# Kernel optimization log

Hardware: AMD Instinct MI355X
Metric: run time of the kernel (lower is better)

Reference implementation:

```python
import jax, jax.numpy as jnp
import numpy as np

H = 8          # n_heads
LORA_SCALE = 1.0


def _lora(x, down, up):
    # nn.Linear convention: y = x @ W.T ; down:[r,in], up:[out,r]
    return (x @ down.T) @ up.T


def setup_inputs() -> dict:
    key = jax.random.key(0)
    ks = jax.random.split(key, 16)
    B, S, D, R = 4, 2048, 640, 4
    std = 1.0 / np.sqrt(D)
    inp = {
        "hidden_states": jax.random.normal(ks[0], (B, S, D), jnp.float32),
        "wq": jax.random.normal(ks[1], (D, D), jnp.float32) * std,
        "wk": jax.random.normal(ks[2], (D, D), jnp.float32) * std,
        "wv": jax.random.normal(ks[3], (D, D), jnp.float32) * std,
        "wo": jax.random.normal(ks[4], (D, D), jnp.float32) * std,
        "bo": jax.random.normal(ks[5], (D,), jnp.float32) * 0.02,
        "q_down": jax.random.normal(ks[6], (R, D), jnp.float32) * (1.0 / R),
        "q_up": jax.random.normal(ks[7], (D, R), jnp.float32) * 0.02,
        "k_down": jax.random.normal(ks[8], (R, D), jnp.float32) * (1.0 / R),
        "k_up": jax.random.normal(ks[9], (D, R), jnp.float32) * 0.02,
        "v_down": jax.random.normal(ks[10], (R, D), jnp.float32) * (1.0 / R),
        "v_up": jax.random.normal(ks[11], (D, R), jnp.float32) * 0.02,
        "o_down": jax.random.normal(ks[12], (R, D), jnp.float32) * (1.0 / R),
        "o_up": jax.random.normal(ks[13], (D, R), jnp.float32) * 0.02,
    }
    return inp


def reference(hidden_states, wq, wk, wv, wo, bo,
              q_down, q_up, k_down, k_up, v_down, v_up, o_down, o_up):
    B, S, D = hidden_states.shape
    hd = D // H
    sm_scale = 1.0 / np.sqrt(hd)

    x = hidden_states  # self-attention: encoder_hidden_states = hidden_states
    q = x @ wq.T + LORA_SCALE * _lora(x, q_down, q_up)
    k = x @ wk.T + LORA_SCALE * _lora(x, k_down, k_up)
    v = x @ wv.T + LORA_SCALE * _lora(x, v_down, v_up)

    # head_to_batch_dim: [B,S,D] -> [B,H,S,hd]
    q = q.reshape(B, S, H, hd).transpose(0, 2, 1, 3)
    k = k.reshape(B, S, H, hd).transpose(0, 2, 1, 3)
    v = v.reshape(B, S, H, hd).transpose(0, 2, 1, 3)

    # get_attention_scores: baddbmm(beta=0, alpha=1/sqrt(hd)) + softmax
    scores = jnp.einsum("bhqd,bhkd->bhqk", q, k) * sm_scale
    probs = jax.nn.softmax(scores, axis=-1)
    attn_out = jnp.einsum("bhqk,bhkd->bhqd", probs, v)

    # batch_to_head_dim: [B,H,S,hd] -> [B,S,D]
    attn_out = attn_out.transpose(0, 2, 1, 3).reshape(B, S, D)

    # out projection (with bias) + LoRA on the pre-projection hidden states
    out = attn_out @ wo.T + bo + LORA_SCALE * _lora(attn_out, o_down, o_up)
    # to_out[1] is dropout -> identity at eval
    return out
```

## Files before the change

kernel.cpp:

```cpp
#include <hip/hip_runtime.h>

typedef unsigned short u16;
typedef unsigned int u32;
typedef unsigned long long u64;

typedef __bf16 bf16x8 __attribute__((ext_vector_type(8)));
typedef float f32x4 __attribute__((ext_vector_type(4)));
typedef float f32x16 __attribute__((ext_vector_type(16)));

__device__ __forceinline__ float b2f(u16 u) {
    union { u32 i; float f; } c; c.i = ((u32)u) << 16; return c.f;
}
__device__ __forceinline__ u16 f2b(float f) {
    union { float f; u32 i; } c; c.f = f;
    u32 r = c.i + 0x7fffu + ((c.i >> 16) & 1u);
    return (u16)(r >> 16);
}
__device__ __forceinline__ u32 cvt_pk_bf16(float a, float b) {
    u32 r;
    asm("v_cvt_pk_bf16_f32 %0, %1, %2" : "=v"(r) : "v"(a), "v"(b));
    return r;
}
__device__ __forceinline__ float fexp2(float x) {
    float r;
    asm("v_exp_f32 %0, %1" : "=v"(r) : "v"(x));
    return r;
}

__device__ __forceinline__ f32x4 mfma16(bf16x8 a, bf16x8 b, f32x4 c) {
    return __builtin_amdgcn_mfma_f32_16x16x32_bf16(a, b, c, 0, 0, 0);
}
__device__ __forceinline__ f32x16 mfma32(bf16x8 a, bf16x8 b, f32x16 c) {
    return __builtin_amdgcn_mfma_f32_32x32x16_bf16(a, b, c, 0, 0, 0);
}

__device__ __forceinline__ void lds_cp16(const u16* gsrc, u16* ldst) {
    __builtin_amdgcn_global_load_lds(
        (const __attribute__((address_space(1))) u32*)gsrc,
        (__attribute__((address_space(3))) u32*)ldst, 16, 0, 0);
}

struct ConvJobs {
    const float* s[4];
    u16* d[4];
};

__global__ __launch_bounds__(256) void convert_w(ConvJobs J) {
    int j = blockIdx.y;
    int i = blockIdx.x * 256 + threadIdx.x;
    float4 v = ((const float4*)J.s[j])[i];
    ushort4 o;
    o.x = f2b(v.x); o.y = f2b(v.y); o.z = f2b(v.z); o.w = f2b(v.w);
    ((ushort4*)J.d[j])[i] = o;
}

__global__ __launch_bounds__(256) void fuse_x(const float* __restrict__ x,
                                              const float* __restrict__ qd,
                                              const float* __restrict__ kd,
                                              const float* __restrict__ vd,
                                              u16* __restrict__ xb,
                                              float* __restrict__ T) {
    int m = blockIdx.x * 4 + (threadIdx.x >> 6);
    int lane = threadIdx.x & 63;
    const float* row = x + (size_t)m * 640;
    u16* orow = xb + (size_t)m * 640;
    float acc[12];
#pragma unroll
    for (int r = 0; r < 12; ++r) acc[r] = 0.f;
#pragma unroll
    for (int ii = 0; ii < 10; ++ii) {
        int i = lane + ii * 64;
        float a = row[i];
        orow[i] = f2b(a);
#pragma unroll
        for (int r = 0; r < 4; ++r) {
            acc[r]     += a * qd[r * 640 + i];
            acc[4 + r] += a * kd[r * 640 + i];
            acc[8 + r] += a * vd[r * 640 + i];
        }
    }
#pragma unroll
    for (int off = 32; off > 0; off >>= 1)
#pragma unroll
        for (int r = 0; r < 12; ++r) acc[r] += __shfl_xor(acc[r], off);
    if (lane == 0) {
#pragma unroll
        for (int p = 0; p < 3; ++p) {
            float4* t = (float4*)(T + ((size_t)p * 8192 + m) * 4);
            *t = make_float4(acc[p * 4], acc[p * 4 + 1], acc[p * 4 + 2], acc[p * 4 + 3]);
        }
    }
}

__global__ __launch_bounds__(256) void lora_down_o(const u16* __restrict__ A,
                                                   const float* __restrict__ dn,
                                                   float* __restrict__ T) {
    int m = blockIdx.x * 4 + (threadIdx.x >> 6);
    int lane = threadIdx.x & 63;
    const u16* arow = A + (size_t)m * 640;
    float a0 = 0.f, a1 = 0.f, a2 = 0.f, a3 = 0.f;
    for (int i = lane; i < 640; i += 64) {
        float a = b2f(arow[i]);
        a0 += a * dn[i];
        a1 += a * dn[640 + i];
        a2 += a * dn[1280 + i];
        a3 += a * dn[1920 + i];
    }
#pragma unroll
    for (int off = 32; off > 0; off >>= 1) {
        a0 += __shfl_xor(a0, off);
        a1 += __shfl_xor(a1, off);
        a2 += __shfl_xor(a2, off);
        a3 += __shfl_xor(a3, off);
    }
    if (lane == 0) {
        float4* t = (float4*)(T + (size_t)m * 4);
        *t = make_float4(a0, a1, a2, a3);
    }
}

struct QkvPtrs {
    const u16* W[3];
    const float* up[3];
    void* out[3];
    float scale[3];
};

__global__ __launch_bounds__(256) void gemm_bt(const u16* __restrict__ A, QkvPtrs P,
                                               const float* __restrict__ T,
                                               const float* __restrict__ bias, int mode) {
    int z = blockIdx.z;
    const u16* W = P.W[z];
    const float* up = P.up[z];
    const float scl = P.scale[z];
    const float* Tz = T + (size_t)z * 8192 * 4;
    int m0 = blockIdx.x * 128, n0 = blockIdx.y * 128;
    int tid = threadIdx.x, lane = tid & 63, wid = tid >> 6;
    int g = lane >> 4, l15 = lane & 15;
    __shared__ __align__(16) u16 As[128 * 32];
    __shared__ __align__(16) u16 Bs[128 * 32];
    f32x4 acc[4][4] = {};
    int wm = (wid & 1) * 64, wn = (wid >> 1) * 64;

    for (int k0 = 0; k0 < 640; k0 += 32) {
        __syncthreads();
#pragma unroll
        for (int it = 0; it < 2; ++it) {
            int f = tid + it * 256;
            int r = f >> 2, c = f & 3;
            lds_cp16(A + (size_t)(m0 + r) * 640 + k0 + c * 8, As + f * 8);
            lds_cp16(W + (size_t)(n0 + r) * 640 + k0 + c * 8, Bs + f * 8);
        }
        __syncthreads();
        bf16x8 af[4], bfv[4];
#pragma unroll
        for (int t = 0; t < 4; ++t) {
            af[t] = *(const bf16x8*)(As + (wm + t * 16 + l15) * 32 + g * 8);
            bfv[t] = *(const bf16x8*)(Bs + (wn + t * 16 + l15) * 32 + g * 8);
        }
#pragma unroll
        for (int i = 0; i < 4; ++i)
#pragma unroll
            for (int j = 0; j < 4; ++j)
                acc[i][j] = mfma16(af[i], bfv[j], acc[i][j]);
    }

    float4 upv[4];
    float bv[4];
#pragma unroll
    for (int j = 0; j < 4; ++j) {
        int n = n0 + wn + j * 16 + l15;
        upv[j] = *(const float4*)(up + n * 4);
        bv[j] = mode ? bias[n] : 0.f;
    }
    float* outf = (float*)P.out[z];
    u16* outb = (u16*)P.out[z];
#pragma unroll
    for (int i = 0; i < 4; ++i) {
#pragma unroll
        for (int r = 0; r < 4; ++r) {
            int m = m0 + wm + i * 16 + g * 4 + r;
            const float4 tv = *(const float4*)(Tz + (size_t)m * 4);
#pragma unroll
            for (int j = 0; j < 4; ++j) {
                int n = n0 + wn + j * 16 + l15;
                float v = acc[i][j][r] + tv.x * upv[j].x + tv.y * upv[j].y +
                          tv.z * upv[j].z + tv.w * upv[j].w + bv[j];
                if (mode) {
                    outf[(size_t)m * 640 + n] = v;
                } else {
                    int bb = m >> 11, s = m & 2047;
                    int h = n / 80, d = n - h * 80;
                    outb[(((size_t)bb * 8 + h) * 2048 + s) * 80 + d] = f2b(v * scl);
                }
            }
        }
    }
}

__global__ __launch_bounds__(256) void transpose_v(const u16* __restrict__ Vin,
                                                   u16* __restrict__ Vout) {
    __shared__ u32 lds32[64 * 41];
    int bh = blockIdx.y;
    int s0 = blockIdx.x * 64;
    int tid = threadIdx.x;
    const u16* in = Vin + (size_t)bh * 2048 * 80;
    u16* out = Vout + (size_t)bh * 96 * 2048;

    for (int t = tid; t < 640; t += 256) {
        int s = t / 10, c = t - s * 10;
        uint4 v = *(const uint4*)(in + (size_t)(s0 + s) * 80 + c * 8);
        u32* p = lds32 + s * 41 + c * 4;
        p[0] = v.x; p[1] = v.y; p[2] = v.z; p[3] = v.w;
    }
    __syncthreads();
    for (int t = tid; t < 640; t += 256) {
        int d = t >> 3, c8 = t & 7;
        int dp = d >> 1, hi = d & 1;
        u16 vals[8];
#pragma unroll
        for (int j = 0; j < 8; ++j) {
            u32 w = lds32[(c8 * 8 + j) * 41 + dp];
            vals[j] = hi ? (u16)(w >> 16) : (u16)(w & 0xffff);
        }
        u16* dst = out + (size_t)d * 2048 + s0 + (c8 >> 1) * 16 + (c8 & 1) * 4;
        *(uint2*)dst = *(const uint2*)(vals);
        *(uint2*)(dst + 8) = *(const uint2*)(vals + 4);
    }
    for (int t = tid; t < 1024; t += 256) {
        int r = t >> 6, c = t & 63;
        out[(size_t)(80 + r) * 2048 + s0 + c] = (r == 0) ? 0x3F80 : 0;
    }
}

__global__ __launch_bounds__(512) void flash_attn(const u16* __restrict__ Q,
                                                  const u16* __restrict__ K,
                                                  const u16* __restrict__ Vt_g,
                                                  u16* __restrict__ O) {
    int bh = blockIdx.y;
    int q0 = blockIdx.x * 256;
    int tid = threadIdx.x;
    int lane = tid & 63, wid = tid >> 6, l31 = lane & 31, h2 = lane >> 5;
    const size_t base = (size_t)bh * 2048 * 80;
    const size_t vbase = (size_t)bh * 96 * 2048;

    __shared__ __align__(16) u16 lds[2 * 5632 + 2 * 7200];
    u16* Ks0 = lds;
    u16* Vt0 = lds + 11264;

    bf16x8 qf[5];
    {
        int qrow = q0 + wid * 32 + l31;
#pragma unroll
        for (int ks = 0; ks < 5; ++ks)
            qf[ks] = *(const bf16x8*)(Q + base + (size_t)qrow * 80 + ks * 16 + h2 * 8);
    }

    f32x16 oa[3] = {};
    const float C2 = 17.312340490667562f;

    auto stage = [&](int buf, int kt) {
#pragma unroll
        for (int it = 0; it < 4; ++it) {
            int c = tid + it * 512;
            if (c < 704) {
                int row = c / 11, col = c - row * 11;
                lds_cp16(K + base + (size_t)(kt + row) * 80 + col * 8,
                         Ks0 + buf * 5632 + c * 8);
            } else if (c < 1600) {
                int t = c - 704;
                int row = t / 9, col = t - row * 9;
                lds_cp16(Vt_g + vbase + (size_t)row * 2048 + kt + col * 8,
                         Vt0 + buf * 7200 + t * 8);
            }
        }
    };

    stage(0, 0);
    __syncthreads();

    for (int i = 0; i < 32; ++i) {
        int cur = i & 1;
        if (i < 31) stage(cur ^ 1, (i + 1) * 64);

        const u16* ks = Ks0 + cur * 5632;
        const u16* vt = Vt0 + cur * 7200;

#pragma unroll
        for (int kk2 = 0; kk2 < 2; ++kk2) {
            f32x16 s = {};
#pragma unroll
            for (int ks5 = 0; ks5 < 5; ++ks5) {
                bf16x8 kf = *(const bf16x8*)(ks + (kk2 * 32 + l31) * 88 + ks5 * 16 + h2 * 8);
                s = mfma32(kf, qf[ks5], s);
            }
            u32 d[8];
#pragma unroll
            for (int j = 0; j < 8; ++j)
                d[j] = cvt_pk_bf16(fexp2(s[2 * j] - C2), fexp2(s[2 * j + 1] - C2));
#pragma unroll
            for (int sl = 0; sl < 2; ++sl) {
                union { u32 w[4]; bf16x8 v; } pa;
                pa.w[0] = d[4 * sl + 0];
                pa.w[1] = d[4 * sl + 1];
                pa.w[2] = d[4 * sl + 2];
                pa.w[3] = d[4 * sl + 3];
#pragma unroll
                for (int nt = 0; nt < 3; ++nt) {
                    bf16x8 vf = *(const bf16x8*)(vt + (nt * 32 + l31) * 72 +
                                                 kk2 * 32 + sl * 16 + h2 * 8);
                    oa[nt] = mfma32(pa.v, vf, oa[nt]);
                }
            }
        }
        __syncthreads();
    }

    int b = bh >> 3, h = bh & 7;
    float inv[16];
#pragma unroll
    for (int reg = 0; reg < 16; ++reg)
        inv[reg] = 1.f / __shfl(oa[2][reg], (lane & 32) + 16, 64);
#pragma unroll
    for (int nt = 0; nt < 3; ++nt) {
        int vd = nt * 32 + l31;
        if (vd < 80) {
#pragma unroll
            for (int reg = 0; reg < 16; ++reg) {
                int q = q0 + wid * 32 + (reg & 3) + 8 * (reg >> 2) + 4 * h2;
                O[((size_t)(b * 2048 + q)) * 640 + h * 80 + vd] = f2b(oa[nt][reg] * inv[reg]);
            }
        }
    }
}

extern "C" void kernel_launch(void* const* d_in, const int* in_sizes, int n_in,
                              void* d_out, int out_size, void* d_ws, size_t ws_size,
                              hipStream_t stream) {
    const float* x      = (const float*)d_in[0];
    const float* wq     = (const float*)d_in[1];
    const float* wk     = (const float*)d_in[2];
    const float* wv     = (const float*)d_in[3];
    const float* wo     = (const float*)d_in[4];
    const float* bo     = (const float*)d_in[5];
    const float* q_down = (const float*)d_in[6];
    const float* q_up   = (const float*)d_in[7];
    const float* k_down = (const float*)d_in[8];
    const float* k_up   = (const float*)d_in[9];
    const float* v_down = (const float*)d_in[10];
    const float* v_up   = (const float*)d_in[11];
    const float* o_down = (const float*)d_in[12];
    const float* o_up   = (const float*)d_in[13];

    char* ws = (char*)d_ws;
    u16* xb    = (u16*)(ws);
    u16* vT_ws = (u16*)(ws);
    u16* wbv   = (u16*)(ws + 10485760);
    u16* wbq   = (u16*)(ws + 11304960);
    u16* wbk   = (u16*)(ws + 12124160);
    u16* wbo   = (u16*)(ws + 12943360);
    u16* q_ws  = (u16*)(ws + 13762560);
    u16* k_ws  = (u16*)(ws + 24248320);
    u16* v_ws  = (u16*)(ws + 34734080);
    u16* attn  = (u16*)(ws + 45219840);
    float* Tq  = (float*)(ws + 55705600);
    float* To  = (float*)(ws + 56098816);

    ConvJobs cj;
    cj.s[0] = wq; cj.d[0] = wbq;
    cj.s[1] = wk; cj.d[1] = wbk;
    cj.s[2] = wv; cj.d[2] = wbv;
    cj.s[3] = wo; cj.d[3] = wbo;
    convert_w<<<dim3(400, 4), 256, 0, stream>>>(cj);

    fuse_x<<<2048, 256, 0, stream>>>(x, q_down, k_down, v_down, xb, Tq);

    QkvPtrs pq;
    pq.W[0] = wbq; pq.W[1] = wbk; pq.W[2] = wbv;
    pq.up[0] = q_up; pq.up[1] = k_up; pq.up[2] = v_up;
    pq.out[0] = q_ws; pq.out[1] = k_ws; pq.out[2] = v_ws;
    pq.scale[0] = 0.11180339887498949f * 1.4426950408889634f;
    pq.scale[1] = 1.0f;
    pq.scale[2] = 1.0f;
    gemm_bt<<<dim3(64, 5, 3), 256, 0, stream>>>(xb, pq, Tq, bo, 0);

    transpose_v<<<dim3(32, 32), 256, 0, stream>>>(v_ws, vT_ws);

    flash_attn<<<dim3(8, 32), 512, 0, stream>>>(q_ws, k_ws, vT_ws, attn);

    lora_down_o<<<2048, 256, 0, stream>>>(attn, o_down, To);

    QkvPtrs po;
    po.W[0] = wbo; po.W[1] = wbo; po.W[2] = wbo;
    po.up[0] = o_up; po.up[1] = o_up; po.up[2] = o_up;
    po.out[0] = d_out; po.out[1] = d_out; po.out[2] = d_out;
    po.scale[0] = 1.0f; po.scale[1] = 1.0f; po.scale[2] = 1.0f;
    gemm_bt<<<dim3(64, 5, 1), 256, 0, stream>>>(attn, po, To, bo, 1);
}
```

Before: 240.6 us.

## Write V transposed directly from QKV GEMM epilogue and add MFMA priority hints

The QKV GEMM epilogue for V now writes straight into the transposed, permuted, padded V layout that flash attention expects, which removes the separate transpose_v kernel and its round trip through global memory. The pad rows (a ones row used for the softmax denominator, plus zeros) are filled by extending the weight-convert kernel. This path is taken only when the workspace is large enough. Flash attention also gains s_setprio hints around its MFMA sections to favour matrix issue over the exp work. The transposed stores in the epilogue are strided and poorly coalesced, which could offset what the removed kernel saves.

```diff
diff --git a/kernel.cpp b/kernel.cpp
--- a/kernel.cpp
+++ b/kernel.cpp
@@ -45,13 +45,25 @@
     u16* d[4];
 };
 
-__global__ __launch_bounds__(256) void convert_w(ConvJobs J) {
+__global__ __launch_bounds__(256) void convert_w(ConvJobs J, u16* __restrict__ vt,
+                                                 int do_pad) {
     int j = blockIdx.y;
-    int i = blockIdx.x * 256 + threadIdx.x;
-    float4 v = ((const float4*)J.s[j])[i];
-    ushort4 o;
-    o.x = f2b(v.x); o.y = f2b(v.y); o.z = f2b(v.z); o.w = f2b(v.w);
-    ((ushort4*)J.d[j])[i] = o;
+    int idx = blockIdx.x * 256 + threadIdx.x;
+    if (j < 4) {
+        if (idx >= 102400) return;
+        float4 v = ((const float4*)J.s[j])[idx];
+        ushort4 o;
+        o.x = f2b(v.x); o.y = f2b(v.y); o.z = f2b(v.z); o.w = f2b(v.w);
+        ((ushort4*)J.d[j])[idx] = o;
+    } else if (do_pad) {
+        int q = idx * 4;
+        int bh = q >> 15;
+        int rem = q & 32767;
+        int row = rem >> 11, col = rem & 2047;
+        u16 val = (row == 0) ? (u16)0x3F80 : (u16)0;
+        ushort4 o = make_ushort4(val, val, val, val);
+        *(ushort4*)(vt + ((size_t)bh * 96 + 80 + row) * 2048 + col) = o;
+    }
 }
 
 __global__ __launch_bounds__(256) void fuse_x(const float* __restrict__ x,
@@ -124,15 +136,17 @@
     const float* up[3];
     void* out[3];
     float scale[3];
+    int mode[3];
 };
 
 __global__ __launch_bounds__(256) void gemm_bt(const u16* __restrict__ A, QkvPtrs P,
                                                const float* __restrict__ T,
-                                               const float* __restrict__ bias, int mode) {
+                                               const float* __restrict__ bias) {
     int z = blockIdx.z;
     const u16* W = P.W[z];
     const float* up = P.up[z];
     const float scl = P.scale[z];
+    const int md = P.mode[z];
     const float* Tz = T + (size_t)z * 8192 * 4;
     int m0 = blockIdx.x * 128, n0 = blockIdx.y * 128;
     int tid = threadIdx.x, lane = tid & 63, wid = tid >> 6;
@@ -171,7 +185,7 @@
     for (int j = 0; j < 4; ++j) {
         int n = n0 + wn + j * 16 + l15;
         upv[j] = *(const float4*)(up + n * 4);
-        bv[j] = mode ? bias[n] : 0.f;
+        bv[j] = (md == 1) ? bias[n] : 0.f;
     }
     float* outf = (float*)P.out[z];
     u16* outb = (u16*)P.out[z];
@@ -186,12 +200,17 @@
                 int n = n0 + wn + j * 16 + l15;
                 float v = acc[i][j][r] + tv.x * upv[j].x + tv.y * upv[j].y +
                           tv.z * upv[j].z + tv.w * upv[j].w + bv[j];
-                if (mode) {
+                if (md == 1) {
                     outf[(size_t)m * 640 + n] = v;
+                } else if (md == 0) {
+                    int bb = m >> 11, s = m & 2047;
+                    int h = n / 80, d = n - h * 80;
+                    outb[(((size_t)bb * 8 + h) * 2048 + s) * 80 + d] = f2b(v * scl);
                 } else {
                     int bb = m >> 11, s = m & 2047;
                     int h = n / 80, d = n - h * 80;
-                    outb[(((size_t)bb * 8 + h) * 2048 + s) * 80 + d] = f2b(v * scl);
+                    int sp = (s & ~12) | ((s & 4) << 1) | ((s & 8) >> 1);
+                    outb[(((size_t)bb * 8 + h) * 96 + d) * 2048 + sp] = f2b(v);
                 }
             }
         }
@@ -289,15 +308,18 @@
 #pragma unroll
         for (int kk2 = 0; kk2 < 2; ++kk2) {
             f32x16 s = {};
+            __builtin_amdgcn_s_setprio(1);
 #pragma unroll
             for (int ks5 = 0; ks5 < 5; ++ks5) {
                 bf16x8 kf = *(const bf16x8*)(ks + (kk2 * 32 + l31) * 88 + ks5 * 16 + h2 * 8);
                 s = mfma32(kf, qf[ks5], s);
             }
+            __builtin_amdgcn_s_setprio(0);
             u32 d[8];
 #pragma unroll
             for (int j = 0; j < 8; ++j)
                 d[j] = cvt_pk_bf16(fexp2(s[2 * j] - C2), fexp2(s[2 * j + 1] - C2));
+            __builtin_amdgcn_s_setprio(1);
 #pragma unroll
             for (int sl = 0; sl < 2; ++sl) {
                 union { u32 w[4]; bf16x8 v; } pa;
@@ -312,6 +334,7 @@
                     oa[nt] = mfma32(pa.v, vf, oa[nt]);
                 }
             }
+            __builtin_amdgcn_s_setprio(0);
         }
         __syncthreads();
     }
@@ -354,7 +377,6 @@
 
     char* ws = (char*)d_ws;
     u16* xb    = (u16*)(ws);
-    u16* vT_ws = (u16*)(ws);
     u16* wbv   = (u16*)(ws + 10485760);
     u16* wbq   = (u16*)(ws + 11304960);
     u16* wbk   = (u16*)(ws + 12124160);
@@ -366,25 +388,34 @@
     float* Tq  = (float*)(ws + 55705600);
     float* To  = (float*)(ws + 56098816);
 
+    const size_t vt_off = 56360960;
+    const size_t vt_need = vt_off + 12582912 + 16384;
+    const bool direct_vt = (ws_size >= vt_need);
+    u16* vT_ws = direct_vt ? (u16*)(ws + vt_off)
+                           : (u16*)(ws);
+
     ConvJobs cj;
     cj.s[0] = wq; cj.d[0] = wbq;
     cj.s[1] = wk; cj.d[1] = wbk;
     cj.s[2] = wv; cj.d[2] = wbv;
     cj.s[3] = wo; cj.d[3] = wbo;
-    convert_w<<<dim3(400, 4), 256, 0, stream>>>(cj);
+    convert_w<<<dim3(1024, 5), 256, 0, stream>>>(cj, vT_ws, direct_vt ? 1 : 0);
 
     fuse_x<<<2048, 256, 0, stream>>>(x, q_down, k_down, v_down, xb, Tq);
 
     QkvPtrs pq;
     pq.W[0] = wbq; pq.W[1] = wbk; pq.W[2] = wbv;
     pq.up[0] = q_up; pq.up[1] = k_up; pq.up[2] = v_up;
-    pq.out[0] = q_ws; pq.out[1] = k_ws; pq.out[2] = v_ws;
+    pq.out[0] = q_ws; pq.out[1] = k_ws;
+    pq.out[2] = direct_vt ? (void*)vT_ws : (void*)v_ws;
     pq.scale[0] = 0.11180339887498949f * 1.4426950408889634f;
     pq.scale[1] = 1.0f;
     pq.scale[2] = 1.0f;
-    gemm_bt<<<dim3(64, 5, 3), 256, 0, stream>>>(xb, pq, Tq, bo, 0);
-
-    transpose_v<<<dim3(32, 32), 256, 0, stream>>>(v_ws, vT_ws);
+    pq.mode[0] = 0; pq.mode[1] = 0; pq.mode[2] = direct_vt ? 2 : 0;
+    gemm_bt<<<dim3(64, 5, 3), 256, 0, stream>>>(xb, pq, Tq, bo);
+
+    if (!direct_vt)
+        transpose_v<<<dim3(32, 32), 256, 0, stream>>>(v_ws, vT_ws);
 
     flash_attn<<<dim3(8, 32), 512, 0, stream>>>(q_ws, k_ws, vT_ws, attn);
 
@@ -395,5 +426,6 @@
     po.up[0] = o_up; po.up[1] = o_up; po.up[2] = o_up;
     po.out[0] = d_out; po.out[1] = d_out; po.out[2] = d_out;
     po.scale[0] = 1.0f; po.scale[1] = 1.0f; po.scale[2] = 1.0f;
-    gemm_bt<<<dim3(64, 5, 1), 256, 0, stream>>>(attn, po, To, bo, 1);
-}
+    po.mode[0] = 1; po.mode[1] = 1; po.mode[2] = 1;
+    gemm_bt<<<dim3(64, 5, 1), 256, 0, stream>>>(attn, po, To, bo);
+}
```

Measured after the change: 241.8 us. About the same (+0.5%).

## Triple-buffer projection GEMM loads and raise wave priority around attention MFMAs

Applied to the files above, without the earlier changes.

The projection GEMM now uses a three-stage LDS ring. It issues global-to-LDS copies two K-steps ahead and uses a vmcnt wait plus a single barrier per iteration, replacing the previous two-barrier, load-then-compute loop. This is meant to hide global load latency behind the MFMA work, at the cost of three times the LDS for those tiles. The attention kernel also wraps its MFMA sections in s_setprio so waves doing matrix work get issue priority over waves doing exp and conversion, to encourage overlap across waves.

```diff
diff --git a/kernel.cpp b/kernel.cpp
--- a/kernel.cpp
+++ b/kernel.cpp
@@ -137,33 +137,54 @@
     int m0 = blockIdx.x * 128, n0 = blockIdx.y * 128;
     int tid = threadIdx.x, lane = tid & 63, wid = tid >> 6;
     int g = lane >> 4, l15 = lane & 15;
-    __shared__ __align__(16) u16 As[128 * 32];
-    __shared__ __align__(16) u16 Bs[128 * 32];
+    __shared__ __align__(16) u16 As[3][4096];
+    __shared__ __align__(16) u16 Bs[3][4096];
     f32x4 acc[4][4] = {};
     int wm = (wid & 1) * 64, wn = (wid >> 1) * 64;
 
-    for (int k0 = 0; k0 < 640; k0 += 32) {
-        __syncthreads();
-#pragma unroll
-        for (int it = 0; it < 2; ++it) {
-            int f = tid + it * 256;
-            int r = f >> 2, c = f & 3;
-            lds_cp16(A + (size_t)(m0 + r) * 640 + k0 + c * 8, As + f * 8);
-            lds_cp16(W + (size_t)(n0 + r) * 640 + k0 + c * 8, Bs + f * 8);
-        }
-        __syncthreads();
+    int r0 = tid >> 2, cb = (tid & 3) * 8;
+    const u16* pA = A + (size_t)(m0 + r0) * 640 + cb;
+    const u16* pB = W + (size_t)(n0 + r0) * 640 + cb;
+
+    auto stage = [&](int buf, int k0) {
+        u16* da = &As[buf][tid * 8];
+        u16* db = &Bs[buf][tid * 8];
+        lds_cp16(pA + k0, da);
+        lds_cp16(pA + 40960 + k0, da + 2048);
+        lds_cp16(pB + k0, db);
+        lds_cp16(pB + 40960 + k0, db + 2048);
+    };
+    auto compute = [&](int cur) {
+        const u16* as = &As[cur][0];
+        const u16* bs = &Bs[cur][0];
         bf16x8 af[4], bfv[4];
 #pragma unroll
-        for (int t = 0; t < 4; ++t) {
-            af[t] = *(const bf16x8*)(As + (wm + t * 16 + l15) * 32 + g * 8);
-            bfv[t] = *(const bf16x8*)(Bs + (wn + t * 16 + l15) * 32 + g * 8);
+        for (int q4 = 0; q4 < 4; ++q4) {
+            af[q4]  = *(const bf16x8*)(as + (wm + q4 * 16 + l15) * 32 + g * 8);
+            bfv[q4] = *(const bf16x8*)(bs + (wn + q4 * 16 + l15) * 32 + g * 8);
         }
 #pragma unroll
         for (int i = 0; i < 4; ++i)
 #pragma unroll
             for (int j = 0; j < 4; ++j)
                 acc[i][j] = mfma16(af[i], bfv[j], acc[i][j]);
-    }
+    };
+
+    stage(0, 0);
+    stage(1, 32);
+    int cur = 0;
+    for (int t = 0; t < 19; ++t) {
+        asm volatile("s_waitcnt vmcnt(4)" ::: "memory");
+        __builtin_amdgcn_s_barrier();
+        asm volatile("" ::: "memory");
+        if (t < 18) stage((cur == 0) ? 2 : cur - 1, (t + 2) * 32);
+        compute(cur);
+        cur = (cur == 2) ? 0 : cur + 1;
+    }
+    asm volatile("s_waitcnt vmcnt(0)" ::: "memory");
+    __builtin_amdgcn_s_barrier();
+    asm volatile("" ::: "memory");
+    compute(cur);
 
     float4 upv[4];
     float bv[4];
@@ -289,15 +310,18 @@
 #pragma unroll
         for (int kk2 = 0; kk2 < 2; ++kk2) {
             f32x16 s = {};
+            __builtin_amdgcn_s_setprio(1);
 #pragma unroll
             for (int ks5 = 0; ks5 < 5; ++ks5) {
                 bf16x8 kf = *(const bf16x8*)(ks + (kk2 * 32 + l31) * 88 + ks5 * 16 + h2 * 8);
                 s = mfma32(kf, qf[ks5], s);
             }
+            __builtin_amdgcn_s_setprio(0);
             u32 d[8];
 #pragma unroll
             for (int j = 0; j < 8; ++j)
                 d[j] = cvt_pk_bf16(fexp2(s[2 * j] - C2), fexp2(s[2 * j + 1] - C2));
+            __builtin_amdgcn_s_setprio(1);
 #pragma unroll
             for (int sl = 0; sl < 2; ++sl) {
                 union { u32 w[4]; bf16x8 v; } pa;
@@ -312,6 +336,7 @@
                     oa[nt] = mfma32(pa.v, vf, oa[nt]);
                 }
             }
+            __builtin_amdgcn_s_setprio(0);
         }
         __syncthreads();
     }
```

Result: no change. 239.4 us (-0.5%).
